# Kernel optimization log

Hardware: AMD Instinct MI355X
Metric: run time of the kernel (lower is better)

## Reference

```python
import jax, jax.numpy as jnp
import numpy as np

# model dims
B_, S_, D_ = 2, 2048, 1024
D_STATE, EXPAND, HEADDIM, CHUNK, NGROUPS = 128, 2, 64, 64, 1
D_INNER = EXPAND * D_
NHEADS = D_INNER // HEADDIM  # 32 ssd heads
D_PROJ = 2 * D_INNER + 2 * NGROUPS * D_STATE + NHEADS  # 4384
H_, KV_, HD_ = 16, 4, 64  # attention heads / kv heads / head dim
ROPE_DIMS = 16
MLP_DIM = int(3.0 * D_)


def _rmsnorm(x, w=None, eps=1e-5):
    y = x * jax.lax.rsqrt(jnp.mean(x * x, axis=-1, keepdims=True) + eps)
    return y * w if w is not None else y


def _layernorm(x, w, b, eps=1e-5):
    m = jnp.mean(x, axis=-1, keepdims=True)
    v = jnp.mean((x - m) ** 2, axis=-1, keepdims=True)
    return (x - m) * jax.lax.rsqrt(v + eps) * w + b


def _segsum(x):
    # (..., T) -> (..., T, T) lower-tri cumulative sums, -inf above diag
    T = x.shape[-1]
    i = jnp.arange(T)
    xx = jnp.where(i[:, None] > i[None, :], jnp.broadcast_to(x[..., None], x.shape + (T,)), 0.0)
    s = jnp.cumsum(xx, axis=-2)
    return jnp.where(i[:, None] >= i[None, :], s, -jnp.inf)


def _ssd_chunked(x, A, B, C, chunk):
    # x:(b,s,h,p) A:(b,s,h) B,C:(b,s,g,n)
    b, s, h, p = x.shape
    g, n = B.shape[2], B.shape[3]
    if g < h:
        B = jnp.repeat(B, h // g, axis=2)
        C = jnp.repeat(C, h // g, axis=2)
    c = s // chunk
    x = x.reshape(b, c, chunk, h, p)
    A = A.reshape(b, c, chunk, h).transpose(0, 3, 1, 2)  # b h c l
    B = B.reshape(b, c, chunk, h, n)
    C = C.reshape(b, c, chunk, h, n)
    L = jnp.exp(_segsum(A))
    Y_diag = jnp.einsum('bclhn,bcshn,bhcls,bcshp->bclhp', C, B, L, x)
    A_cum = jnp.cumsum(A, axis=-1)
    decay_states = jnp.exp(A_cum[..., -1:] - A_cum)
    states = jnp.einsum('bclhn,bhcl,bclhp->bchpn', B, decay_states, x)
    decay_chunk = jnp.exp(_segsum(jnp.pad(A_cum[..., -1], ((0, 0), (0, 0), (1, 0)))))
    new_states = jnp.einsum('bhzc,bchpn->bzhpn', decay_chunk[:, :, :c, 1:c + 1], states)
    Y_off = jnp.einsum('bclhn,bchpn,bhcl->bclhp', C, new_states, jnp.exp(A_cum))
    return (Y_diag + Y_off).reshape(b, s, h, p)


def _rope_cos_sin(s, rd, base=10000.0):
    inv = 1.0 / base ** (jnp.arange(0, rd, 2, dtype=jnp.float32) / rd)
    f = jnp.outer(jnp.arange(s, dtype=jnp.float32), inv)  # (s, rd/2)
    return jnp.cos(f)[None, :, None, :], jnp.sin(f)[None, :, None, :]


def _apply_rope(x, cos, sin, rd):
    xr, xp = x[..., :rd], x[..., rd:]
    half = rd // 2
    x1, x2 = xr[..., :half], xr[..., half:]
    xr = jnp.concatenate([x1 * cos + x2 * sin, -x1 * sin + x2 * cos], axis=-1)
    return jnp.concatenate([xr, xp], axis=-1)


def _mamba_block(x, mnorm_w, in_w, out_w, Dp, dt_b, A_log, Bn_w, Cn_w):
    b, s, _ = x.shape
    h = _rmsnorm(x, mnorm_w)
    zxbcdt = h @ in_w.T
    z, xs, Bc, Cc, dt = jnp.split(
        zxbcdt,
        [D_INNER, 2 * D_INNER, 2 * D_INNER + NGROUPS * D_STATE, 2 * D_INNER + 2 * NGROUPS * D_STATE],
        axis=-1)
    dt = jax.nn.softplus(dt + dt_b)  # (b,s,nheads)
    A = -jnp.exp(A_log)  # (nheads,)
    xs = xs.reshape(b, s, NHEADS, HEADDIM)
    Bc = _rmsnorm(Bc.reshape(b, s, NGROUPS, D_STATE), Bn_w)
    Cc = _rmsnorm(Cc.reshape(b, s, NGROUPS, D_STATE), Cn_w)
    y = _ssd_chunked(xs * dt[..., None], A[None, None, :] * dt, Bc, Cc, CHUNK)
    y = y + xs * Dp[None, None, :, None]
    y = y * jax.nn.silu(z).reshape(b, s, NHEADS, HEADDIM)
    return x + y.reshape(b, s, D_INNER) @ out_w.T


def _attn_block(x, ln1_w, ln1_b, cq_w, ck_w, cv_w, cproj_w, q_gain, ln2_w, ln2_b, fc_w, proj_w):
    b, s, d = x.shape
    h = _layernorm(x, ln1_w, ln1_b)
    q = (h @ cq_w.T).reshape(b, s, H_, HD_)
    k = (h @ ck_w.T).reshape(b, s, KV_, HD_)
    v = (h @ cv_w.T).reshape(b, s, KV_, HD_)
    eps = jnp.finfo(x.dtype).eps
    q = _rmsnorm(q, eps=eps)
    k = _rmsnorm(k, eps=eps)
    cos, sin = _rope_cos_sin(s, ROPE_DIMS)
    q = _apply_rope(q, cos, sin, ROPE_DIMS)
    k = _apply_rope(k, cos, sin, ROPE_DIMS)
    q = q * q_gain[None, None, :, None]
    rep = H_ // KV_
    k = jnp.repeat(k, rep, axis=2)
    v = jnp.repeat(v, rep, axis=2)
    scores = jnp.einsum('bqhd,bkhd->bhqk', q, k) / np.float32(np.sqrt(HD_))
    i = jnp.arange(s)
    scores = jnp.where(i[:, None] >= i[None, :], scores, -jnp.inf)
    w = jax.nn.softmax(scores, axis=-1)
    y = jnp.einsum('bhqk,bkhd->bqhd', w, v).reshape(b, s, d)
    x = x + y @ cproj_w.T
    h = _layernorm(x, ln2_w, ln2_b)
    return x + jax.nn.silu(h @ fc_w.T) @ proj_w.T


def setup_inputs() -> dict:
    key = jax.random.key(0)
    ks = jax.random.split(key, 16)
    rn = lambda k, shp, sc=0.02: (jax.random.normal(k, shp, dtype=jnp.float32) * sc)
    return {
        'x': jax.random.normal(ks[0], (B_, S_, D_), dtype=jnp.float32),
        'mnorm_w': jnp.ones((D_,), jnp.float32),
        'in_proj_w': rn(ks[1], (D_PROJ, D_)),
        'out_proj_w': rn(ks[2], (D_, D_INNER)),
        'D_param': jnp.ones((NHEADS,), jnp.float32),
        'dt_bias': rn(ks[3], (NHEADS,), 0.1),
        'A_log': jnp.log(0.5 + jax.random.uniform(ks[4], (NHEADS,), dtype=jnp.float32) * 0.5),
        'Bn_w': jnp.ones((D_STATE,), jnp.float32),
        'Cn_w': jnp.ones((D_STATE,), jnp.float32),
        'ln1_w': jnp.ones((D_,), jnp.float32),
        'ln1_b': jnp.zeros((D_,), jnp.float32),
        'cq_w': rn(ks[5], (D_, D_)),
        'ck_w': rn(ks[6], (KV_ * HD_, D_)),
        'cv_w': rn(ks[7], (KV_ * HD_, D_)),
        'cproj_w': rn(ks[8], (D_, D_)),
        'q_gain': jnp.full((H_,), 5.25, jnp.float32),
        'ln2_w': jnp.ones((D_,), jnp.float32),
        'ln2_b': jnp.zeros((D_,), jnp.float32),
        'fc_w': rn(ks[9], (MLP_DIM, D_)),
        'proj_w': rn(ks[10], (D_, MLP_DIM)),
    }


def reference(x, mnorm_w, in_proj_w, out_proj_w, D_param, dt_bias, A_log, Bn_w, Cn_w,
              ln1_w, ln1_b, cq_w, ck_w, cv_w, cproj_w, q_gain, ln2_w, ln2_b, fc_w, proj_w):
    x = _mamba_block(x, mnorm_w, in_proj_w, out_proj_w, D_param, dt_bias, A_log, Bn_w, Cn_w)
    x = _attn_block(x, ln1_w, ln1_b, cq_w, ck_w, cv_w, cproj_w, q_gain, ln2_w, ln2_b, fc_w, proj_w)
    return x
```

## Files before the change

### kernel.cpp

```cpp
#include <hip/hip_runtime.h>
#include <hip/hip_bf16.h>
#include <math.h>

#define B_    2
#define S_    2048
#define D_    1024
#define DI    2048
#define NH    32
#define HD    64
#define DS    128
#define CH    64
#define NC    32
#define DP    4384
#define HATT  16
#define KVH   4
#define RD    16
#define MLP   3072
#define ROWS  (B_*S_)
#define PSB   (ROWS*288)

typedef __bf16 bf16;
typedef __bf16 bf16x8 __attribute__((ext_vector_type(8)));
typedef __bf16 bf16x4 __attribute__((ext_vector_type(4)));
typedef float  f32x4  __attribute__((ext_vector_type(4)));

__device__ __forceinline__ void async_copy16(const void* g, void* l) {
  __builtin_amdgcn_global_load_lds(
      (const __attribute__((address_space(1))) unsigned int*)g,
      (__attribute__((address_space(3))) unsigned int*)l, 16, 0, 0);
}

__device__ __forceinline__ float waveReduceSum(float v) {
#pragma unroll
  for (int off = 32; off > 0; off >>= 1) v += __shfl_down(v, off, 64);
  return v;
}

template<int NW>
__device__ __forceinline__ float blockReduceSum(float v, float* sh) {
  v = waveReduceSum(v);
  int lane = threadIdx.x & 63, wid = threadIdx.x >> 6;
  if (lane == 0) sh[wid] = v;
  __syncthreads();
  float s = 0.f;
#pragma unroll
  for (int i = 0; i < NW; i++) s += sh[i];
  __syncthreads();
  return s;
}

struct CastSeg { const float* src; bf16* dst; int nval; int ntot; int blk0; };
struct CastArgs { CastSeg seg[8]; };

__global__ __launch_bounds__(256) void castw_all(CastArgs a) {
  int blk = blockIdx.x;
  int si = 0;
#pragma unroll
  for (int i = 1; i < 8; i++) if (blk >= a.seg[i].blk0) si = i;
  CastSeg s = a.seg[si];
  int i = ((blk - s.blk0) * 256 + threadIdx.x) * 4;
  if (i >= s.ntot) return;
  float4 v = {0.f, 0.f, 0.f, 0.f};
  if (i < s.nval) v = *(const float4*)(s.src + i);
  bf16x4 o;
  o[0] = (bf16)v.x; o[1] = (bf16)v.y; o[2] = (bf16)v.z; o[3] = (bf16)v.w;
  *(bf16x4*)(s.dst + i) = o;
}

__global__ __launch_bounds__(256) void rmsnorm_k(const float* __restrict__ x,
                                                 const float* __restrict__ w,
                                                 bf16* __restrict__ y, int n) {
  __shared__ float sh[4];
  size_t row = blockIdx.x;
  const float* xr = x + row * n;
  bf16* yr = y + row * n;
  float ss = 0.f;
  for (int i = threadIdx.x; i < n; i += 256) { float v = xr[i]; ss += v * v; }
  ss = blockReduceSum<4>(ss, sh);
  float inv = rsqrtf(ss / n + 1e-5f);
  for (int i = threadIdx.x; i < n; i += 256) yr[i] = (bf16)(xr[i] * inv * w[i]);
}

template<int ACT, typename OT>
__global__ __launch_bounds__(256) void gemm_mfma(const bf16* __restrict__ A,
                                                 const bf16* __restrict__ W,
                                                 const float* __restrict__ R,
                                                 OT* __restrict__ C,
                                                 int M, int N, int K) {
  __shared__ bf16 lds[3 * 8192];
  int tid = threadIdx.x, lane = tid & 63, wave = tid >> 6;
  int mt = M >> 7;
  int bid = blockIdx.x;
  int bm = (bid % mt) * 128, bn = (bid / mt) * 128;
  const bf16* gA0 = A + (size_t)(bm + wave * 32 + (lane >> 2)) * K + (lane & 3) * 8;
  const bf16* gA1 = gA0 + (size_t)16 * K;
  const bf16* gW0 = W + (size_t)(bn + wave * 32 + (lane >> 2)) * K + (lane & 3) * 8;
  const bf16* gW1 = gW0 + (size_t)16 * K;
  int sA = wave * 1024;
  int fr = lane & 15, fq = lane >> 4;
  int wm = wave >> 1, wn = wave & 1;
  int rdA = (wm * 64 + fr) * 32 + fq * 8;
  int rdW = (wn * 64 + fr) * 32 + fq * 8;
  f32x4 acc[4][4] = {};
  {
    bf16* bA = lds + sA;
    bf16* bW = lds + 4096 + sA;
    async_copy16(gA0, bA);  async_copy16(gA1, bA + 512);
    async_copy16(gW0, bW);  async_copy16(gW1, bW + 512);
  }
  int cur = 0, nxt = 1;
  int nsteps = K >> 5;
  for (int t = 0; t < nsteps; t++) {
    if (t + 1 < nsteps) {
      int off = (t + 1) * 32;
      bf16* bA = lds + nxt * 8192 + sA;
      bf16* bW = lds + nxt * 8192 + 4096 + sA;
      async_copy16(gA0 + off, bA);  async_copy16(gA1 + off, bA + 512);
      async_copy16(gW0 + off, bW);  async_copy16(gW1 + off, bW + 512);
      asm volatile("s_waitcnt vmcnt(4)" ::: "memory");
    } else {
      asm volatile("s_waitcnt vmcnt(0)" ::: "memory");
    }
    __builtin_amdgcn_sched_barrier(0);
    __builtin_amdgcn_s_barrier();
    __builtin_amdgcn_sched_barrier(0);
    const bf16* cA = lds + cur * 8192;
    const bf16* cW = cA + 4096;
    bf16x8 af[4], bfr[4];
#pragma unroll
    for (int mi = 0; mi < 4; mi++) af[mi] = *(const bf16x8*)(cA + rdA + mi * 512);
#pragma unroll
    for (int ni = 0; ni < 4; ni++) bfr[ni] = *(const bf16x8*)(cW + rdW + ni * 512);
    __builtin_amdgcn_s_setprio(1);
#pragma unroll
    for (int mi = 0; mi < 4; mi++)
#pragma unroll
      for (int ni = 0; ni < 4; ni++)
        acc[mi][ni] = __builtin_amdgcn_mfma_f32_16x16x32_bf16(af[mi], bfr[ni], acc[mi][ni], 0, 0, 0);
    __builtin_amdgcn_s_setprio(0);
    cur = nxt; nxt = nxt + 1; if (nxt == 3) nxt = 0;
  }
#pragma unroll
  for (int mi = 0; mi < 4; mi++) {
    int row = bm + wm * 64 + mi * 16 + fq * 4;
#pragma unroll
    for (int ni = 0; ni < 4; ni++) {
      int col = bn + wn * 64 + ni * 16 + fr;
      if (col < N) {
#pragma unroll
        for (int r = 0; r < 4; r++) {
          float v = acc[mi][ni][r];
          if (ACT == 1) v = v / (1.f + __expf(-v));
          if (R) v += R[(size_t)(row + r) * N + col];
          C[(size_t)(row + r) * N + col] = (OT)v;
        }
      }
    }
  }
}

__global__ __launch_bounds__(256) void gemm_sk(const bf16* __restrict__ A,
                                               const bf16* __restrict__ W,
                                               bf16* __restrict__ P,
                                               int M, int N, int K, int kchunk) {
  __shared__ bf16 lds[3 * 8192];
  int tid = threadIdx.x, lane = tid & 63, wave = tid >> 6;
  int mt = M >> 7;
  int bid = blockIdx.x;
  int bm = (bid % mt) * 128, bn = (bid / mt) * 128;
  int ks = blockIdx.z;
  int kbeg = ks * kchunk;
  const bf16* gA0 = A + (size_t)(bm + wave * 32 + (lane >> 2)) * K + kbeg + (lane & 3) * 8;
  const bf16* gA1 = gA0 + (size_t)16 * K;
  const bf16* gW0 = W + (size_t)(bn + wave * 32 + (lane >> 2)) * K + kbeg + (lane & 3) * 8;
  const bf16* gW1 = gW0 + (size_t)16 * K;
  int sA = wave * 1024;
  int fr = lane & 15, fq = lane >> 4;
  int wm = wave >> 1, wn = wave & 1;
  int rdA = (wm * 64 + fr) * 32 + fq * 8;
  int rdW = (wn * 64 + fr) * 32 + fq * 8;
  f32x4 acc[4][4] = {};
  {
    bf16* bA = lds + sA;
    bf16* bW = lds + 4096 + sA;
    async_copy16(gA0, bA);  async_copy16(gA1, bA + 512);
    async_copy16(gW0, bW);  async_copy16(gW1, bW + 512);
  }
  int cur = 0, nxt = 1;
  int nsteps = kchunk >> 5;
  for (int t = 0; t < nsteps; t++) {
    if (t + 1 < nsteps) {
      int off = (t + 1) * 32;
      bf16* bA = lds + nxt * 8192 + sA;
      bf16* bW = lds + nxt * 8192 + 4096 + sA;
      async_copy16(gA0 + off, bA);  async_copy16(gA1 + off, bA + 512);
      async_copy16(gW0 + off, bW);  async_copy16(gW1 + off, bW + 512);
      asm volatile("s_waitcnt vmcnt(4)" ::: "memory");
    } else {
      asm volatile("s_waitcnt vmcnt(0)" ::: "memory");
    }
    __builtin_amdgcn_sched_barrier(0);
    __builtin_amdgcn_s_barrier();
    __builtin_amdgcn_sched_barrier(0);
    const bf16* cA = lds + cur * 8192;
    const bf16* cW = cA + 4096;
    bf16x8 af[4], bfr[4];
#pragma unroll
    for (int mi = 0; mi < 4; mi++) af[mi] = *(const bf16x8*)(cA + rdA + mi * 512);
#pragma unroll
    for (int ni = 0; ni < 4; ni++) bfr[ni] = *(const bf16x8*)(cW + rdW + ni * 512);
    __builtin_amdgcn_s_setprio(1);
#pragma unroll
    for (int mi = 0; mi < 4; mi++)
#pragma unroll
      for (int ni = 0; ni < 4; ni++)
        acc[mi][ni] = __builtin_amdgcn_mfma_f32_16x16x32_bf16(af[mi], bfr[ni], acc[mi][ni], 0, 0, 0);
    __builtin_amdgcn_s_setprio(0);
    cur = nxt; nxt = nxt + 1; if (nxt == 3) nxt = 0;
  }
  bf16* Pp = P + (size_t)ks * M * N;
#pragma unroll
  for (int mi = 0; mi < 4; mi++) {
    int row = bm + wm * 64 + mi * 16 + fq * 4;
#pragma unroll
    for (int ni = 0; ni < 4; ni++) {
      int col = bn + wn * 64 + ni * 16 + fr;
#pragma unroll
      for (int r = 0; r < 4; r++)
        Pp[(size_t)(row + r) * N + col] = (bf16)acc[mi][ni][r];
    }
  }
}

__global__ __launch_bounds__(256) void reduce_ln2(const bf16* __restrict__ p0,
                                                  const bf16* __restrict__ p1,
                                                  const float* __restrict__ res,
                                                  const float* __restrict__ w,
                                                  const float* __restrict__ b,
                                                  float* __restrict__ xo,
                                                  bf16* __restrict__ ho) {
  __shared__ float sh[4];
  size_t o = (size_t)blockIdx.x * 1024;
  int i = threadIdx.x * 4;
  bf16x4 a = *(const bf16x4*)(p0 + o + i);
  bf16x4 c = *(const bf16x4*)(p1 + o + i);
  f32x4 rv = *(const f32x4*)(res + o + i);
  f32x4 v;
  float s = 0.f, s2 = 0.f;
#pragma unroll
  for (int j = 0; j < 4; j++) {
    v[j] = (float)a[j] + (float)c[j] + rv[j];
    s += v[j]; s2 += v[j] * v[j];
  }
  s  = blockReduceSum<4>(s,  sh);
  s2 = blockReduceSum<4>(s2, sh);
  float mean = s / 1024.f;
  float var  = s2 / 1024.f - mean * mean;
  float inv  = rsqrtf(var + 1e-5f);
  f32x4 wv = *(const f32x4*)(w + i);
  f32x4 bv = *(const f32x4*)(b + i);
  *(f32x4*)(xo + o + i) = v;
  bf16x4 hv;
#pragma unroll
  for (int j = 0; j < 4; j++) hv[j] = (bf16)((v[j] - mean) * inv * wv[j] + bv[j]);
  *(bf16x4*)(ho + o + i) = hv;
}

__global__ __launch_bounds__(256) void reduce_out3(const bf16* __restrict__ p0,
                                                   const bf16* __restrict__ p1,
                                                   const bf16* __restrict__ p2,
                                                   const float* __restrict__ res,
                                                   float* __restrict__ out) {
  int i = (blockIdx.x * 256 + threadIdx.x) * 4;
  bf16x4 a = *(const bf16x4*)(p0 + i);
  bf16x4 c = *(const bf16x4*)(p1 + i);
  bf16x4 d = *(const bf16x4*)(p2 + i);
  f32x4 v = *(const f32x4*)(res + i);
#pragma unroll
  for (int j = 0; j < 4; j++) v[j] += (float)a[j] + (float)c[j] + (float)d[j];
  *(f32x4*)(out + i) = v;
}

__global__ __launch_bounds__(256) void reduce_qkv(const bf16* __restrict__ P,
                                                  const float* __restrict__ q_gain,
                                                  bf16* __restrict__ q,
                                                  bf16* __restrict__ k,
                                                  bf16* __restrict__ v) {
  __shared__ float buf[1536];
  size_t row = blockIdx.x;
  size_t o = row * 1536;
  const bf16* p0 = P + o;
  const bf16* p1 = P + (size_t)ROWS * 1536 + o;
  int tid = threadIdx.x;
  for (int i = tid; i < 384; i += 256) {
    bf16x4 a = *(const bf16x4*)(p0 + i * 4);
    bf16x4 c = *(const bf16x4*)(p1 + i * 4);
    f32x4 vv;
#pragma unroll
    for (int j = 0; j < 4; j++) vv[j] = (float)a[j] + (float)c[j];
    *(f32x4*)(buf + i * 4) = vv;
  }
  __syncthreads();
  int lane = tid & 63, w = tid >> 6;
  int s = (int)(row & (S_ - 1));
  int ri = lane & 7;
  float rinv = __expf(-(float)ri * (0.125f * 9.210340371976184f));
  float ang = (float)s * rinv;
  float cs = cosf(ang), sn = sinf(ang);
#pragma unroll
  for (int j = 0; j < 6; j++) {
    int hh = w * 6 + j;
    float val = buf[hh * 64 + lane];
    if (hh < 20) {
      float ss = val * val;
#pragma unroll
      for (int off = 32; off > 0; off >>= 1) ss += __shfl_xor(ss, off, 64);
      val *= rsqrtf(ss / 64.f + 1.1920929e-7f);
      float other = __shfl_xor(val, 8, 64);
      float res = val;
      if (lane < RD) res = (lane < 8) ? (val * cs + other * sn) : (val * cs - other * sn);
      if (hh < 16) {
        res *= q_gain[hh];
        q[row * (HATT * HD) + hh * HD + lane] = (bf16)res;
      } else {
        k[row * (KVH * HD) + (hh - 16) * HD + lane] = (bf16)res;
      }
    } else {
      v[row * (KVH * HD) + (hh - 20) * HD + lane] = (bf16)val;
    }
  }
}

__global__ __launch_bounds__(512, 2) void gemm256_inproj(const bf16* __restrict__ A,
                                                         const bf16* __restrict__ W,
                                                         bf16* __restrict__ zt,
                                                         bf16* __restrict__ xt,
                                                         bf16* __restrict__ bcdtP) {
  __shared__ bf16 lds[3 * 16384];
  int tid = threadIdx.x;
  int lane = tid & 63, w = tid >> 6;
  int fr = lane & 15, fq = lane >> 4;
  int rdswz = (fq ^ (fr & 3)) * 8;
  int sswz = (lane & 3) ^ ((lane >> 2) & 3);
  int bid = blockIdx.x;
  if (bid < 256) {
    int sb = (bid & 7) * 32 + (bid >> 3);
    int bm = (sb & 15) * 256;
    int bn = (sb >> 4) * 256;
    int wm = w >> 2, wn = w & 3;
    int srow = w * 32 + (lane >> 2);
    const bf16* gA = A + (size_t)(bm + srow) * 1024 + sswz * 8;
    const bf16* gW = W + (size_t)(bn + srow) * 1024 + sswz * 8;
    int sbase = w * 1024;
    f32x4 acc[8][4] = {};
    {
      bf16* bA = lds + sbase;
      bf16* bB = lds + 8192 + sbase;
      async_copy16(gA, bA);
      async_copy16(gA + 16 * 1024, bA + 512);
      async_copy16(gW, bB);
      async_copy16(gW + 16 * 1024, bB + 512);
    }
    int cur = 0, nxt = 1;
    for (int t = 0; t < 32; t++) {
      if (t + 1 < 32) {
        const bf16* ga = gA + (t + 1) * 32;
        const bf16* gw = gW + (t + 1) * 32;
        bf16* bA = lds + nxt * 16384 + sbase;
        bf16* bB = lds + nxt * 16384 + 8192 + sbase;
        async_copy16(ga, bA);
        async_copy16(ga + 16 * 1024, bA + 512);
        async_copy16(gw, bB);
        async_copy16(gw + 16 * 1024, bB + 512);
        asm volatile("s_waitcnt vmcnt(4)" ::: "memory");
      } else {
        asm volatile("s_waitcnt vmcnt(0)" ::: "memory");
      }
      __builtin_amdgcn_sched_barrier(0);
      __builtin_amdgcn_s_barrier();
      __builtin_amdgcn_sched_barrier(0);
      const bf16* cA = lds + cur * 16384;
      const bf16* cB = cA + 8192;
      bf16x8 af[8], bfv[4];
#pragma unroll
      for (int mi = 0; mi < 8; mi++)
        af[mi] = *(const bf16x8*)(cA + (wm * 128 + mi * 16 + fr) * 32 + rdswz);
#pragma unroll
      for (int ni = 0; ni < 4; ni++)
        bfv[ni] = *(const bf16x8*)(cB + (wn * 64 + ni * 16 + fr) * 32 + rdswz);
      __builtin_amdgcn_s_setprio(1);
#pragma unroll
      for (int mi = 0; mi < 8; mi++)
#pragma unroll
        for (int ni = 0; ni < 4; ni++)
          acc[mi][ni] = __builtin_amdgcn_mfma_f32_16x16x32_bf16(af[mi], bfv[ni], acc[mi][ni], 0, 0, 0);
      __builtin_amdgcn_s_setprio(0);
      cur = nxt; nxt = nxt + 1; if (nxt == 3) nxt = 0;
    }
    bf16* base = (bn < 2048) ? zt : xt;
    int bq = bm >> 11, bmS = bm & 2047;
    bf16* Ts = lds;
#pragma unroll 1
    for (int g = 0; g < 4; g++) {
      __syncthreads();
      if (wn == g) {
#pragma unroll
        for (int mi = 0; mi < 8; mi++)
#pragma unroll
          for (int ni = 0; ni < 4; ni++) {
            bf16x4 o;
#pragma unroll
            for (int r = 0; r < 4; r++) o[r] = (bf16)acc[mi][ni][r];
            *(bf16x4*)(Ts + (ni * 16 + fr) * 264 + wm * 128 + mi * 16 + fq * 4) = o;
          }
      }
      __syncthreads();
      int hh = ((bn & 2047) + g * 64) >> 6;
      bf16* dst = base + ((size_t)(bq * NH + hh) * HD) * S_ + bmS;
#pragma unroll
      for (int i = 0; i < 4; i++) {
        int idx = tid + i * 512;
        int p = idx >> 5, sc = (idx & 31) * 8;
        *(bf16x8*)(dst + (size_t)p * S_ + sc) = *(const bf16x8*)(Ts + p * 264 + sc);
      }
    }
  } else {
    int lb = bid - 256;
    int ks = lb / 96;
    int pos = lb - ks * 96;
    int bm = (pos & 31) * 128;
    int bn = 4096 + (pos >> 5) * 128;
    int kbeg = ks * 512;
    int wm = w >> 1, wn = w & 1;
    int srow = w * 16 + (lane >> 2);
    const bf16* gA = A + (size_t)(bm + srow) * 1024 + kbeg + sswz * 8;
    const bf16* gW = W + (size_t)(bn + srow) * 1024 + kbeg + sswz * 8;
    int sbase = w * 512;
    f32x4 acc[2][4] = {};
    {
      async_copy16(gA, lds + sbase);
      async_copy16(gW, lds + 4096 + sbase);
    }
    int cur = 0, nxt = 1;
    for (int t = 0; t < 16; t++) {
      if (t + 1 < 16) {
        async_copy16(gA + (t + 1) * 32, lds + nxt * 8192 + sbase);
        async_copy16(gW + (t + 1) * 32, lds + nxt * 8192 + 4096 + sbase);
        asm volatile("s_waitcnt vmcnt(2)" ::: "memory");
      } else {
        asm volatile("s_waitcnt vmcnt(0)" ::: "memory");
      }
      __builtin_amdgcn_sched_barrier(0);
      __builtin_amdgcn_s_barrier();
      __builtin_amdgcn_sched_barrier(0);
      const bf16* cA = lds + cur * 8192;
      const bf16* cB = cA + 4096;
      bf16x8 af[2], bfv[4];
#pragma unroll
      for (int mi = 0; mi < 2; mi++)
        af[mi] = *(const bf16x8*)(cA + (wm * 32 + mi * 16 + fr) * 32 + rdswz);
#pragma unroll
      for (int ni = 0; ni < 4; ni++)
        bfv[ni] = *(const bf16x8*)(cB + (wn * 64 + ni * 16 + fr) * 32 + rdswz);
#pragma unroll
      for (int mi = 0; mi < 2; mi++)
#pragma unroll
        for (int ni = 0; ni < 4; ni++)
          acc[mi][ni] = __builtin_amdgcn_mfma_f32_16x16x32_bf16(af[mi], bfv[ni], acc[mi][ni], 0, 0, 0);
      cur = nxt; nxt = nxt + 1; if (nxt == 3) nxt = 0;
    }
    bf16* dst = bcdtP + (size_t)ks * PSB;
#pragma unroll
    for (int mi = 0; mi < 2; mi++) {
      int row = bm + wm * 32 + mi * 16 + fq * 4;
#pragma unroll
      for (int ni = 0; ni < 4; ni++) {
        int col = bn + wn * 64 + ni * 16 + fr;
        if (col < 4384) {
#pragma unroll
          for (int r = 0; r < 4; r++)
            dst[(size_t)(row + r) * 288 + (col - 4096)] = (bf16)acc[mi][ni][r];
        }
      }
    }
  }
}

__global__ __launch_bounds__(256) void t64(const bf16* __restrict__ in, bf16* __restrict__ out,
                                           int istr, size_t io, size_t oo, int n_nt) {
  __shared__ bf16 T[64 * 72];
  int bid = blockIdx.x;
  int st = bid & 31;
  int nt = (bid >> 5) % n_nt;
  int outer = bid / (32 * n_nt);
  const bf16* ip = in + outer * io + (size_t)st * 64 * istr + nt * 64;
  int tid = threadIdx.x;
#pragma unroll
  for (int i = 0; i < 2; i++) {
    int cid = tid + i * 256; int s = cid >> 3, pc = (cid & 7) * 8;
    *(bf16x8*)(T + s * 72 + pc) = *(const bf16x8*)(ip + (size_t)s * istr + pc);
  }
  __syncthreads();
  bf16* op = out + outer * oo + (size_t)nt * 64 * 2048 + st * 64;
#pragma unroll
  for (int i = 0; i < 2; i++) {
    int cid = tid + i * 256; int p = cid >> 3, sc = (cid & 7) * 8;
    bf16x8 o;
#pragma unroll
    for (int j = 0; j < 8; j++) o[j] = T[(sc + j) * 72 + p];
    *(bf16x8*)(op + (size_t)p * 2048 + sc) = o;
  }
}

__global__ __launch_bounds__(64) void ssd_prep(const bf16* __restrict__ bcdtP,
                                               const float* __restrict__ dt_bias,
                                               const float* __restrict__ A_log,
                                               float* __restrict__ dt_c,
                                               float* __restrict__ ddc,
                                               float* __restrict__ ac_c,
                                               float* __restrict__ T_out) {
  int bid = blockIdx.x;
  int c = bid % NC, hh = (bid / NC) % NH, b = bid / (NC * NH);
  int l = threadIdx.x;
  size_t row = (size_t)b * S_ + c * 64 + l;
  float raw = (float)bcdtP[row * 288 + 256 + hh]
            + (float)bcdtP[(size_t)PSB + row * 288 + 256 + hh] + dt_bias[hh];
  float dtv = (raw > 20.f) ? raw : log1pf(__expf(raw));
  float a = -__expf(A_log[hh]) * dtv;
  float ps = a;
#pragma unroll
  for (int off = 1; off < 64; off <<= 1) {
    float t = __shfl_up(ps, off, 64);
    if (l >= off) ps += t;
  }
  float a63 = __shfl(ps, 63, 64);
  size_t o = ((size_t)b * NH + hh) * S_ + c * 64 + l;
  dt_c[o] = dtv;
  ac_c[o] = ps;
  ddc[o] = __expf(a63 - ps) * dtv;
  if (l == 63) T_out[(b * NH + hh) * NC + c] = ps;
}

__global__ __launch_bounds__(128) void bc_norm(const bf16* __restrict__ bcdtP,
                                               const float* __restrict__ Bw,
                                               const float* __restrict__ Cw,
                                               bf16* __restrict__ Bn,
                                               bf16* __restrict__ Cn) {
  __shared__ float shb[2], shc[2];
  size_t row = blockIdx.x;
  int i = threadIdx.x;
  float bv = (float)bcdtP[row * 288 + i] + (float)bcdtP[(size_t)PSB + row * 288 + i];
  float cv = (float)bcdtP[row * 288 + 128 + i] + (float)bcdtP[(size_t)PSB + row * 288 + 128 + i];
  float sb = waveReduceSum(bv * bv);
  float sc = waveReduceSum(cv * cv);
  int lane = threadIdx.x & 63, wid = threadIdx.x >> 6;
  if (lane == 0) { shb[wid] = sb; shc[wid] = sc; }
  __syncthreads();
  float tb = shb[0] + shb[1];
  float tc = shc[0] + shc[1];
  Bn[row * DS + i] = (bf16)(bv * rsqrtf(tb / DS + 1e-5f) * Bw[i]);
  Cn[row * DS + i] = (bf16)(cv * rsqrtf(tc / DS + 1e-5f) * Cw[i]);
}

__global__ __launch_bounds__(256) void ssd_states(const bf16* __restrict__ Xt,
                                                  const bf16* __restrict__ Btr,
                                                  const float* __restrict__ ddc,
                                                  bf16* __restrict__ states) {
  __shared__ bf16 Xs[64 * 72];
  __shared__ bf16 Bs[128 * 72];
  int bid = blockIdx.x;
  int h = bid % NH;
  int c = (bid / NH) % NC;
  int b = bid / (NH * NC);
  int tid = threadIdx.x, lane = tid & 63, w = tid >> 6;
  int fr = lane & 15, fq = lane >> 4;
  const size_t xbase = (size_t)(b * NH + h) * HD * S_ + c * 64;
  const size_t dbase = (size_t)(b * NH + h) * S_ + c * 64;
#pragma unroll
  for (int i = 0; i < 2; i++) {
    int cid = tid + i * 256; int p = cid >> 3, sc = (cid & 7) * 8;
    bf16x8 xv = *(const bf16x8*)(Xt + xbase + (size_t)p * S_ + sc);
    f32x4 d0 = *(const f32x4*)(ddc + dbase + sc);
// ... 152 lines not shown
  for (int pt = 0; pt < 4; pt++)
#pragma unroll
    for (int ks = 0; ks < 4; ks++)
      acc[pt] = __builtin_amdgcn_mfma_f32_16x16x32_bf16(ca[ks],
                  *(const bf16x8*)(BNs + (pt * 16 + fr) * 136 + ks * 32 + fq * 8), acc[pt], 0, 0, 0);
  float dph = Dp[h];
#pragma unroll
  for (int pt = 0; pt < 4; pt++) {
    int p = pt * 16 + fr;
    size_t tb = (xbase + (size_t)p * S_) + w * 16 + fq * 4;
    bf16x4 xs4 = *(const bf16x4*)(Xt + tb);
    bf16x4 z4  = *(const bf16x4*)(Zt + tb);
#pragma unroll
    for (int r = 0; r < 4; r++) {
      int l = w * 16 + fq * 4 + r;
      float yv = acc[pt][r] + (float)xs4[r] * dph;
      float z = (float)z4[r];
      yv *= z / (1.f + __expf(-z));
      ybf[((row0 + l) * NH + h) * HD + p] = (bf16)yv;
    }
  }
}

#define KSTR 72
#define PSTR 72
__global__ __launch_bounds__(256) void attn_mfma(const bf16* __restrict__ q,
                                                 const bf16* __restrict__ k,
                                                 const bf16* __restrict__ vtr,
                                                 bf16* __restrict__ Po,
                                                 float* __restrict__ Ls) {
  __shared__ bf16 Ks[64 * KSTR];
  __shared__ bf16 Vs[64 * KSTR];
  __shared__ bf16 Pl[4][32 * PSTR];
  int c = 39 - blockIdx.x;
  int g = (c < 4) ? 0 : (c < 12) ? 1 : (c < 24) ? 2 : 3;
  int gbase = (g == 0) ? 0 : (g == 1) ? 4 : (g == 2) ? 12 : 24;
  int d = c - gbase;
  int qt = 4 * g + d / (g + 1);
  int sk = d % (g + 1);
  int h = blockIdx.y, b = blockIdx.z;
  int kvh = h >> 2;
  int tid = threadIdx.x, lane = tid & 63, w = tid >> 6;
  int fr = lane & 15, fq = lane >> 4;
  const float SC = 0.18033688011112042f;
  const float M2 = 62.0f;
  int kt0 = sk * 8;
  int ktend = min(kt0 + 8, 2 * qt + 2);
  int qbase = qt * 128 + w * 32;
  int qmaxw = qbase + 31;
  bf16x8 bq[2][2];
#pragma unroll
  for (int qc = 0; qc < 2; qc++)
#pragma unroll
    for (int ks = 0; ks < 2; ks++)
      bq[qc][ks] = *(const bf16x8*)(q + (size_t)(b * S_ + qbase + qc * 16 + fr) * (HATT * HD)
                                      + h * HD + ks * 32 + fq * 8);
  int sr = tid >> 3, sc8 = (tid & 7) * 8;
  const bf16* kg = k + ((size_t)(b * S_) + sr) * (KVH * HD) + kvh * HD + sc8;
  const bf16* vg = vtr + ((size_t)(b * KVH + kvh) * HD + sr) * S_ + sc8;
  bf16x8 krg0, krg1, vrg0, vrg1;
  {
    const bf16* kp = kg + (size_t)kt0 * 64 * (KVH * HD);
    const bf16* vp = vg + (size_t)kt0 * 64;
    krg0 = *(const bf16x8*)(kp);
    krg1 = *(const bf16x8*)(kp + (size_t)32 * (KVH * HD));
    vrg0 = *(const bf16x8*)(vp);
    vrg1 = *(const bf16x8*)(vp + (size_t)32 * S_);
  }
  float lsum[2] = {0.f, 0.f};
  f32x4 yacc[2][4] = {};
  bf16* Plw = Pl[w];
  for (int kt = kt0; kt < ktend; kt++) {
    __syncthreads();
    *(bf16x8*)(&Ks[sr * KSTR + sc8]) = krg0;
    *(bf16x8*)(&Ks[(sr + 32) * KSTR + sc8]) = krg1;
    *(bf16x8*)(&Vs[sr * KSTR + sc8]) = vrg0;
    *(bf16x8*)(&Vs[(sr + 32) * KSTR + sc8]) = vrg1;
    __syncthreads();
    if ((kt + 1) < ktend) {
      const bf16* kp = kg + (size_t)(kt + 1) * 64 * (KVH * HD);
      const bf16* vp = vg + (size_t)(kt + 1) * 64;
      krg0 = *(const bf16x8*)(kp);
      krg1 = *(const bf16x8*)(kp + (size_t)32 * (KVH * HD));
      vrg0 = *(const bf16x8*)(vp);
      vrg1 = *(const bf16x8*)(vp + (size_t)32 * S_);
    }
    if (kt * 64 <= qmaxw) {
      bool nomask = (kt * 64 + 63) <= qbase;
      if (nomask) {
#pragma unroll
        for (int mi = 0; mi < 4; mi++) {
          const bf16* krow = &Ks[(mi * 16 + fr) * KSTR];
          bf16x8 ak0 = *(const bf16x8*)(krow + fq * 8);
          bf16x8 ak1 = *(const bf16x8*)(krow + 32 + fq * 8);
#pragma unroll
          for (int qc = 0; qc < 2; qc++) {
            f32x4 s = {};
            s = __builtin_amdgcn_mfma_f32_16x16x32_bf16(ak0, bq[qc][0], s, 0, 0, 0);
            s = __builtin_amdgcn_mfma_f32_16x16x32_bf16(ak1, bq[qc][1], s, 0, 0, 0);
            bf16x4 pk;
#pragma unroll
            for (int r = 0; r < 4; r++) {
              float p = __builtin_amdgcn_exp2f(s[r] * SC - M2);
              lsum[qc] += p;
              pk[r] = (bf16)p;
            }
            *(bf16x4*)(Plw + (qc * 16 + fr) * PSTR + mi * 16 + fq * 4) = pk;
          }
        }
      } else {
#pragma unroll
        for (int mi = 0; mi < 4; mi++) {
          int s0 = kt * 64 + mi * 16;
          if (s0 > qmaxw) {
            bf16x4 zz = {};
#pragma unroll
            for (int qc = 0; qc < 2; qc++)
              *(bf16x4*)(Plw + (qc * 16 + fr) * PSTR + mi * 16 + fq * 4) = zz;
          } else {
            const bf16* krow = &Ks[(mi * 16 + fr) * KSTR];
            bf16x8 ak0 = *(const bf16x8*)(krow + fq * 8);
            bf16x8 ak1 = *(const bf16x8*)(krow + 32 + fq * 8);
#pragma unroll
            for (int qc = 0; qc < 2; qc++) {
              f32x4 s = {};
              s = __builtin_amdgcn_mfma_f32_16x16x32_bf16(ak0, bq[qc][0], s, 0, 0, 0);
              s = __builtin_amdgcn_mfma_f32_16x16x32_bf16(ak1, bq[qc][1], s, 0, 0, 0);
              int qq = qbase + qc * 16 + fr;
              bf16x4 pk;
#pragma unroll
              for (int r = 0; r < 4; r++) {
                int sp = s0 + fq * 4 + r;
                float p = (sp <= qq) ? __builtin_amdgcn_exp2f(s[r] * SC - M2) : 0.f;
                lsum[qc] += p;
                pk[r] = (bf16)p;
              }
              *(bf16x4*)(Plw + (qc * 16 + fr) * PSTR + mi * 16 + fq * 4) = pk;
            }
          }
        }
      }
#pragma unroll
      for (int ks2 = 0; ks2 < 2; ks2++) {
        bf16x8 bp[2];
#pragma unroll
        for (int qc = 0; qc < 2; qc++)
          bp[qc] = *(const bf16x8*)(Plw + (qc * 16 + fr) * PSTR + ks2 * 32 + fq * 8);
#pragma unroll
        for (int pi = 0; pi < 4; pi++) {
          bf16x8 av = *(const bf16x8*)(&Vs[(pi * 16 + fr) * KSTR + ks2 * 32 + fq * 8]);
#pragma unroll
          for (int qc = 0; qc < 2; qc++)
            yacc[qc][pi] = __builtin_amdgcn_mfma_f32_16x16x32_bf16(av, bp[qc], yacc[qc][pi], 0, 0, 0);
        }
      }
    }
  }
#pragma unroll
  for (int qc = 0; qc < 2; qc++) {
    lsum[qc] += __shfl_xor(lsum[qc], 16, 64);
    lsum[qc] += __shfl_xor(lsum[qc], 32, 64);
    int qrow = qt * 128 + w * 32 + qc * 16 + fr;
    if (fq == 0)
      Ls[((size_t)(b * 16 + h) * 2048 + qrow) * 4 + sk] = lsum[qc];
    bf16* pop = Po + ((((size_t)(b * 16 + h) * 16 + qt) * 4 + sk) * 128
                       + w * 32 + qc * 16 + fr) * 64 + fq * 4;
#pragma unroll
    for (int pi = 0; pi < 4; pi++) {
      bf16x4 o;
#pragma unroll
      for (int r = 0; r < 4; r++) o[r] = (bf16)yacc[qc][pi][r];
      *(bf16x4*)(pop + pi * 16) = o;
    }
  }
}

__global__ __launch_bounds__(256) void attn_red(const bf16* __restrict__ Po,
                                                const float* __restrict__ Ls,
                                                bf16* __restrict__ y2) {
  int row = blockIdx.x;
  int b = row >> 11;
  int qrow = row & 2047;
  int qt = qrow >> 7, r = qrow & 127;
  int nch = (qt >> 2) + 1;
  int t = threadIdx.x;
  int h = t >> 4, e4 = (t & 15) << 2;
  const float* lp = Ls + ((size_t)(b * 16 + h) * 2048 + qrow) * 4;
  float ls = 0.f;
  f32x4 acc = {};
  for (int sk = 0; sk < nch; sk++) {
    ls += lp[sk];
    const bf16* pp = Po + ((((size_t)(b * 16 + h) * 16 + qt) * 4 + sk) * 128 + r) * 64 + e4;
    bf16x4 v = *(const bf16x4*)(pp);
#pragma unroll
    for (int j = 0; j < 4; j++) acc[j] += (float)v[j];
  }
  float inv = 1.f / ls;
  bf16x4 o;
#pragma unroll
  for (int j = 0; j < 4; j++) o[j] = (bf16)(acc[j] * inv);
  *(bf16x4*)(y2 + (size_t)row * 1024 + h * 64 + e4) = o;
}

constexpr size_t OFF_WIN  = 0;
constexpr size_t OFF_WOUT = 9175040;
constexpr size_t OFF_WQKV = 13369344;
constexpr size_t OFF_WCP  = 16515072;
constexpr size_t OFF_WFC  = 18612224;
constexpr size_t OFF_WPR  = 24903680;
constexpr size_t OFF_HBF  = 31195136;
constexpr size_t OFF_BCDT = 39583744;
constexpr size_t OFF_XT   = 41943040;
constexpr size_t OFF_ZT   = 58720256;
constexpr size_t OFF_DTC  = 75497472;
constexpr size_t OFF_DDC  = 76546048;
constexpr size_t OFF_ACC  = 77594624;
constexpr size_t OFF_T    = 78643200;
constexpr size_t OFF_BN   = 78651392;
constexpr size_t OFF_CN   = 79699968;
constexpr size_t OFF_BTR  = 80748544;
constexpr size_t OFF_ST   = 81797120;
constexpr size_t OFF_YBF  = 148905984;
constexpr size_t OFF_X1   = 165683200;
constexpr size_t OFF_P    = OFF_ST;
constexpr size_t OFF_PO   = OFF_ST;
constexpr size_t OFF_LS   = OFF_BCDT;
constexpr size_t OFF_QB   = OFF_XT;
constexpr size_t OFF_KB   = OFF_XT + 8388608;
constexpr size_t OFF_VB   = OFF_XT + 10485760;
constexpr size_t OFF_VTR  = OFF_XT + 12582912;
constexpr size_t OFF_Y2   = OFF_ZT;
constexpr size_t OFF_X2   = 50331648;
constexpr size_t OFF_MLP  = 132128768;

extern "C" void kernel_launch(void* const* d_in, const int* in_sizes, int n_in,
                              void* d_out, int out_size, void* d_ws, size_t ws_size,
                              hipStream_t stream) {
  (void)in_sizes; (void)n_in; (void)out_size; (void)ws_size;
  const float* x        = (const float*)d_in[0];
  const float* mnorm_w  = (const float*)d_in[1];
  const float* in_w     = (const float*)d_in[2];
  const float* out_w    = (const float*)d_in[3];
  const float* Dp       = (const float*)d_in[4];
  const float* dt_bias  = (const float*)d_in[5];
  const float* A_log    = (const float*)d_in[6];
  const float* Bn_w     = (const float*)d_in[7];
  const float* Cn_w     = (const float*)d_in[8];
  const float* ln1_w    = (const float*)d_in[9];
  const float* ln1_b    = (const float*)d_in[10];
  const float* cq_w     = (const float*)d_in[11];
  const float* ck_w     = (const float*)d_in[12];
  const float* cv_w     = (const float*)d_in[13];
  const float* cproj_w  = (const float*)d_in[14];
  const float* q_gain   = (const float*)d_in[15];
  const float* ln2_w    = (const float*)d_in[16];
  const float* ln2_b    = (const float*)d_in[17];
  const float* fc_w     = (const float*)d_in[18];
  const float* proj_w   = (const float*)d_in[19];
  float* out = (float*)d_out;
  char* W8 = (char*)d_ws;

  bf16* w_in   = (bf16*)(W8 + OFF_WIN);
  bf16* w_out  = (bf16*)(W8 + OFF_WOUT);
  bf16* w_qkv  = (bf16*)(W8 + OFF_WQKV);
  bf16* w_cp   = (bf16*)(W8 + OFF_WCP);
  bf16* w_fc   = (bf16*)(W8 + OFF_WFC);
  bf16* w_pr   = (bf16*)(W8 + OFF_WPR);
  bf16* h_bf   = (bf16*)(W8 + OFF_HBF);
  bf16* bcdtP  = (bf16*)(W8 + OFF_ST);
  bf16* Xt     = (bf16*)(W8 + OFF_XT);
  bf16* Zt     = (bf16*)(W8 + OFF_ZT);
  float* dt_c  = (float*)(W8 + OFF_DTC);
  float* ddc   = (float*)(W8 + OFF_DDC);
  float* ac_c  = (float*)(W8 + OFF_ACC);
  float* Tb    = (float*)(W8 + OFF_T);
  bf16* Bn     = (bf16*)(W8 + OFF_BN);
  bf16* Cn     = (bf16*)(W8 + OFF_CN);
  bf16* Btr    = (bf16*)(W8 + OFF_BTR);
  bf16* st     = (bf16*)(W8 + OFF_ST);
  bf16* ybf    = (bf16*)(W8 + OFF_YBF);
  float* x1    = (float*)(W8 + OFF_X1);
  bf16* Pbuf   = (bf16*)(W8 + OFF_P);
  bf16* Po     = (bf16*)(W8 + OFF_PO);
  float* Ls    = (float*)(W8 + OFF_LS);
  bf16* qbf    = (bf16*)(W8 + OFF_QB);
  bf16* kbf    = (bf16*)(W8 + OFF_KB);
  bf16* vbf    = (bf16*)(W8 + OFF_VB);
  bf16* vtr    = (bf16*)(W8 + OFF_VTR);
  bf16* y2     = (bf16*)(W8 + OFF_Y2);
  float* x2    = (float*)(W8 + OFF_X2);
  bf16* mlp    = (bf16*)(W8 + OFF_MLP);

  CastArgs ca;
  ca.seg[0] = { in_w,    w_in,            4489216, 4587520, 0     };
  ca.seg[1] = { out_w,   w_out,           2097152, 2097152, 4480  };
  ca.seg[2] = { cq_w,    w_qkv,           1048576, 1048576, 6528  };
  ca.seg[3] = { ck_w,    w_qkv + 1048576,  262144,  262144, 7552  };
  ca.seg[4] = { cv_w,    w_qkv + 1310720,  262144,  262144, 7808  };
  ca.seg[5] = { cproj_w, w_cp,            1048576, 1048576, 8064  };
  ca.seg[6] = { fc_w,    w_fc,            3145728, 3145728, 9088  };
  ca.seg[7] = { proj_w,  w_pr,            3145728, 3145728, 12160 };
  castw_all<<<15232, 256, 0, stream>>>(ca);

  const size_t PS  = (size_t)ROWS * 1024;

  rmsnorm_k<<<ROWS, 256, 0, stream>>>(x, mnorm_w, h_bf, D_);
  gemm256_inproj<<<448, 512, 0, stream>>>(h_bf, w_in, Zt, Xt, bcdtP);
  ssd_prep<<<B_ * NH * NC, 64, 0, stream>>>(bcdtP, dt_bias, A_log, dt_c, ddc, ac_c, Tb);
  bc_norm<<<ROWS, 128, 0, stream>>>(bcdtP, Bn_w, Cn_w, Bn, Cn);
  t64<<<2 * 2 * 32, 256, 0, stream>>>(Bn, Btr, 128, (size_t)2048 * 128, (size_t)128 * 2048, 2);
  ssd_states<<<B_ * NC * NH, 256, 0, stream>>>(Xt, Btr, ddc, st);
  ssd_scan<<<B_ * NH * 8, 256, 0, stream>>>(st, Tb);
  ssd_out<<<B_ * NC * NH, 256, 0, stream>>>(Cn, Bn, Xt, Zt, dt_c, ac_c, st, Dp, ybf);
  gemm_sk<<<dim3(32 * 8, 1, 2), 256, 0, stream>>>(ybf, w_out, Pbuf, ROWS, D_, DI, 1024);
  reduce_ln2<<<ROWS, 256, 0, stream>>>(Pbuf, Pbuf + PS, x, ln1_w, ln1_b, x1, h_bf);

  gemm_sk<<<dim3(32 * 12, 1, 2), 256, 0, stream>>>(h_bf, w_qkv, Pbuf, ROWS, 1536, D_, 512);
  reduce_qkv<<<ROWS, 256, 0, stream>>>(Pbuf, q_gain, qbf, kbf, vbf);
  t64<<<2 * 4 * 32, 256, 0, stream>>>(vbf, vtr, 256, (size_t)2048 * 256, (size_t)256 * 2048, 4);
  attn_mfma<<<dim3(40, HATT, B_), 256, 0, stream>>>(qbf, kbf, vtr, Po, Ls);
  attn_red<<<ROWS, 256, 0, stream>>>(Po, Ls, y2);
  gemm_sk<<<dim3(32 * 8, 1, 2), 256, 0, stream>>>(y2, w_cp, Pbuf, ROWS, D_, D_, 512);
  reduce_ln2<<<ROWS, 256, 0, stream>>>(Pbuf, Pbuf + PS, x1, ln2_w, ln2_b, x2, h_bf);

  gemm_mfma<1, bf16><<<32 * 24, 256, 0, stream>>>(h_bf, w_fc, nullptr, mlp, ROWS, MLP, D_);
  gemm_sk<<<dim3(32 * 8, 1, 3), 256, 0, stream>>>(mlp, w_pr, Pbuf, ROWS, D_, MLP, 1024);
  reduce_out3<<<ROWS, 256, 0, stream>>>(Pbuf, Pbuf + PS, Pbuf + 2 * PS, x2, out);
}
```

Before: 496.0 us.

## Replace 128x128 GEMMs with unified 256x256 split-K MFMA kernel with swizzled LDS

Replaces the separate 128x128-tile gemm_mfma and gemm_sk kernels with a single 256x256-tile, 512-thread gemm256 kernel. The new kernel uses an XOR-swizzled LDS layout and remaps block IDs across the 8 XCDs. Split-K factors change: the out-proj, c_proj and MLP down-proj GEMMs now use 4 partials, and the MLP up-proj has SiLU fused and no split-K. The reductions are updated to sum 4 partials. The larger tiles aim for more operand reuse per load and fewer launches per wave. The cost is 96KB of LDS per block, which limits occupancy, and a larger partial buffer that must be allocated with enough room.

```diff
diff --git a/kernel.cpp b/kernel.cpp
--- a/kernel.cpp
+++ b/kernel.cpp
@@ -81,120 +81,52 @@
   for (int i = threadIdx.x; i < n; i += 256) yr[i] = (bf16)(xr[i] * inv * w[i]);
 }
 
-template<int ACT, typename OT>
-__global__ __launch_bounds__(256) void gemm_mfma(const bf16* __restrict__ A,
-                                                 const bf16* __restrict__ W,
-                                                 const float* __restrict__ R,
-                                                 OT* __restrict__ C,
-                                                 int M, int N, int K) {
-  __shared__ bf16 lds[3 * 8192];
-  int tid = threadIdx.x, lane = tid & 63, wave = tid >> 6;
-  int mt = M >> 7;
+template<int ACT>
+__global__ __launch_bounds__(512, 2) void gemm256(const bf16* __restrict__ A,
+                                                  const bf16* __restrict__ W,
+                                                  bf16* __restrict__ P,
+                                                  int N, int K, int kchunk, int nwg) {
+  __shared__ bf16 lds[3 * 16384];
+  int tid = threadIdx.x;
+  int lane = tid & 63, w = tid >> 6;
+  int fr = lane & 15, fq = lane >> 4;
+  int rdswz = (fq ^ (fr & 3)) * 8;
+  int sswz = (lane & 3) ^ ((lane >> 2) & 3);
   int bid = blockIdx.x;
-  int bm = (bid % mt) * 128, bn = (bid / mt) * 128;
-  const bf16* gA0 = A + (size_t)(bm + wave * 32 + (lane >> 2)) * K + (lane & 3) * 8;
-  const bf16* gA1 = gA0 + (size_t)16 * K;
-  const bf16* gW0 = W + (size_t)(bn + wave * 32 + (lane >> 2)) * K + (lane & 3) * 8;
-  const bf16* gW1 = gW0 + (size_t)16 * K;
-  int sA = wave * 1024;
-  int fr = lane & 15, fq = lane >> 4;
-  int wm = wave >> 1, wn = wave & 1;
-  int rdA = (wm * 64 + fr) * 32 + fq * 8;
-  int rdW = (wn * 64 + fr) * 32 + fq * 8;
-  f32x4 acc[4][4] = {};
+  int cpx = nwg >> 3;
+  bid = (bid & 7) * cpx + (bid >> 3);
+  int bm = (bid & 15) * 256;
+  int rest = bid >> 4;
+  int nt = N >> 8;
+  int bn = (rest % nt) * 256;
+  int ks = rest / nt;
+  int kbeg = ks * kchunk;
+  int wm = w >> 2, wn = w & 3;
+  int srow = w * 32 + (lane >> 2);
+  const bf16* gA = A + (size_t)(bm + srow) * K + kbeg + sswz * 8;
+  const bf16* gW = W + (size_t)(bn + srow) * K + kbeg + sswz * 8;
+  int sbase = w * 1024;
+  f32x4 acc[8][4] = {};
   {
-    bf16* bA = lds + sA;
-    bf16* bW = lds + 4096 + sA;
-    async_copy16(gA0, bA);  async_copy16(gA1, bA + 512);
-    async_copy16(gW0, bW);  async_copy16(gW1, bW + 512);
-  }
-  int cur = 0, nxt = 1;
-  int nsteps = K >> 5;
-  for (int t = 0; t < nsteps; t++) {
-    if (t + 1 < nsteps) {
-      int off = (t + 1) * 32;
-      bf16* bA = lds + nxt * 8192 + sA;
-      bf16* bW = lds + nxt * 8192 + 4096 + sA;
-      async_copy16(gA0 + off, bA);  async_copy16(gA1 + off, bA + 512);
-      async_copy16(gW0 + off, bW);  async_copy16(gW1 + off, bW + 512);
-      asm volatile("s_waitcnt vmcnt(4)" ::: "memory");
-    } else {
-      asm volatile("s_waitcnt vmcnt(0)" ::: "memory");
-    }
-    __builtin_amdgcn_sched_barrier(0);
-    __builtin_amdgcn_s_barrier();
-    __builtin_amdgcn_sched_barrier(0);
-    const bf16* cA = lds + cur * 8192;
-    const bf16* cW = cA + 4096;
-    bf16x8 af[4], bfr[4];
-#pragma unroll
-    for (int mi = 0; mi < 4; mi++) af[mi] = *(const bf16x8*)(cA + rdA + mi * 512);
-#pragma unroll
-    for (int ni = 0; ni < 4; ni++) bfr[ni] = *(const bf16x8*)(cW + rdW + ni * 512);
-    __builtin_amdgcn_s_setprio(1);
-#pragma unroll
-    for (int mi = 0; mi < 4; mi++)
-#pragma unroll
-      for (int ni = 0; ni < 4; ni++)
-        acc[mi][ni] = __builtin_amdgcn_mfma_f32_16x16x32_bf16(af[mi], bfr[ni], acc[mi][ni], 0, 0, 0);
-    __builtin_amdgcn_s_setprio(0);
-    cur = nxt; nxt = nxt + 1; if (nxt == 3) nxt = 0;
-  }
-#pragma unroll
-  for (int mi = 0; mi < 4; mi++) {
-    int row = bm + wm * 64 + mi * 16 + fq * 4;
-#pragma unroll
-    for (int ni = 0; ni < 4; ni++) {
-      int col = bn + wn * 64 + ni * 16 + fr;
-      if (col < N) {
-#pragma unroll
-        for (int r = 0; r < 4; r++) {
-          float v = acc[mi][ni][r];
-          if (ACT == 1) v = v / (1.f + __expf(-v));
-          if (R) v += R[(size_t)(row + r) * N + col];
-          C[(size_t)(row + r) * N + col] = (OT)v;
-        }
-      }
-    }
-  }
-}
-
-__global__ __launch_bounds__(256) void gemm_sk(const bf16* __restrict__ A,
-                                               const bf16* __restrict__ W,
-                                               bf16* __restrict__ P,
-                                               int M, int N, int K, int kchunk) {
-  __shared__ bf16 lds[3 * 8192];
-  int tid = threadIdx.x, lane = tid & 63, wave = tid >> 6;
-  int mt = M >> 7;
-  int bid = blockIdx.x;
-  int bm = (bid % mt) * 128, bn = (bid / mt) * 128;
-  int ks = blockIdx.z;
-  int kbeg = ks * kchunk;
-  const bf16* gA0 = A + (size_t)(bm + wave * 32 + (lane >> 2)) * K + kbeg + (lane & 3) * 8;
-  const bf16* gA1 = gA0 + (size_t)16 * K;
-  const bf16* gW0 = W + (size_t)(bn + wave * 32 + (lane >> 2)) * K + kbeg + (lane & 3) * 8;
-  const bf16* gW1 = gW0 + (size_t)16 * K;
-  int sA = wave * 1024;
-  int fr = lane & 15, fq = lane >> 4;
-  int wm = wave >> 1, wn = wave & 1;
-  int rdA = (wm * 64 + fr) * 32 + fq * 8;
-  int rdW = (wn * 64 + fr) * 32 + fq * 8;
-  f32x4 acc[4][4] = {};
-  {
-    bf16* bA = lds + sA;
-    bf16* bW = lds + 4096 + sA;
-    async_copy16(gA0, bA);  async_copy16(gA1, bA + 512);
-    async_copy16(gW0, bW);  async_copy16(gW1, bW + 512);
+    bf16* bA = lds + sbase;
+    bf16* bB = lds + 8192 + sbase;
+    async_copy16(gA, bA);
+    async_copy16(gA + (size_t)16 * K, bA + 512);
+    async_copy16(gW, bB);
+    async_copy16(gW + (size_t)16 * K, bB + 512);
   }
   int cur = 0, nxt = 1;
   int nsteps = kchunk >> 5;
   for (int t = 0; t < nsteps; t++) {
     if (t + 1 < nsteps) {
-      int off = (t + 1) * 32;
-      bf16* bA = lds + nxt * 8192 + sA;
-      bf16* bW = lds + nxt * 8192 + 4096 + sA;
-      async_copy16(gA0 + off, bA);  async_copy16(gA1 + off, bA + 512);
-      async_copy16(gW0 + off, bW);  async_copy16(gW1 + off, bW + 512);
+      const bf16* ga = gA + (t + 1) * 32;
+      const bf16* gw = gW + (t + 1) * 32;
+      bf16* bA = lds + nxt * 16384 + sbase;
+      bf16* bB = lds + nxt * 16384 + 8192 + sbase;
+      async_copy16(ga, bA);
+      async_copy16(ga + (size_t)16 * K, bA + 512);
+      async_copy16(gw, bB);
+      async_copy16(gw + (size_t)16 * K, bB + 512);
       asm volatile("s_waitcnt vmcnt(4)" ::: "memory");
     } else {
       asm volatile("s_waitcnt vmcnt(0)" ::: "memory");
@@ -202,56 +134,61 @@
     __builtin_amdgcn_sched_barrier(0);
     __builtin_amdgcn_s_barrier();
     __builtin_amdgcn_sched_barrier(0);
-    const bf16* cA = lds + cur * 8192;
-    const bf16* cW = cA + 4096;
-    bf16x8 af[4], bfr[4];
-#pragma unroll
-    for (int mi = 0; mi < 4; mi++) af[mi] = *(const bf16x8*)(cA + rdA + mi * 512);
-#pragma unroll
-    for (int ni = 0; ni < 4; ni++) bfr[ni] = *(const bf16x8*)(cW + rdW + ni * 512);
+    const bf16* cA = lds + cur * 16384;
+    const bf16* cB = cA + 8192;
+    bf16x8 af[8], bfv[4];
+#pragma unroll
+    for (int mi = 0; mi < 8; mi++)
+      af[mi] = *(const bf16x8*)(cA + (wm * 128 + mi * 16 + fr) * 32 + rdswz);
+#pragma unroll
+    for (int ni = 0; ni < 4; ni++)
+      bfv[ni] = *(const bf16x8*)(cB + (wn * 64 + ni * 16 + fr) * 32 + rdswz);
     __builtin_amdgcn_s_setprio(1);
 #pragma unroll
-    for (int mi = 0; mi < 4; mi++)
+    for (int mi = 0; mi < 8; mi++)
 #pragma unroll
       for (int ni = 0; ni < 4; ni++)
-        acc[mi][ni] = __builtin_amdgcn_mfma_f32_16x16x32_bf16(af[mi], bfr[ni], acc[mi][ni], 0, 0, 0);
+        acc[mi][ni] = __builtin_amdgcn_mfma_f32_16x16x32_bf16(af[mi], bfv[ni], acc[mi][ni], 0, 0, 0);
     __builtin_amdgcn_s_setprio(0);
     cur = nxt; nxt = nxt + 1; if (nxt == 3) nxt = 0;
   }
-  bf16* Pp = P + (size_t)ks * M * N;
-#pragma unroll
-  for (int mi = 0; mi < 4; mi++) {
-    int row = bm + wm * 64 + mi * 16 + fq * 4;
+  bf16* Pp = P + (size_t)ks * ROWS * N;
+#pragma unroll
+  for (int mi = 0; mi < 8; mi++) {
+    int row = bm + wm * 128 + mi * 16 + fq * 4;
 #pragma unroll
     for (int ni = 0; ni < 4; ni++) {
       int col = bn + wn * 64 + ni * 16 + fr;
 #pragma unroll
-      for (int r = 0; r < 4; r++)
-        Pp[(size_t)(row + r) * N + col] = (bf16)acc[mi][ni][r];
-    }
-  }
-}
-
-__global__ __launch_bounds__(256) void reduce_ln2(const bf16* __restrict__ p0,
-                                                  const bf16* __restrict__ p1,
+      for (int r = 0; r < 4; r++) {
+        float v = acc[mi][ni][r];
+        if (ACT == 1) v = v / (1.f + __expf(-v));
+        Pp[(size_t)(row + r) * N + col] = (bf16)v;
+      }
+    }
+  }
+}
+
+__global__ __launch_bounds__(256) void reduce_ln4(const bf16* __restrict__ P,
                                                   const float* __restrict__ res,
                                                   const float* __restrict__ w,
                                                   const float* __restrict__ b,
                                                   float* __restrict__ xo,
                                                   bf16* __restrict__ ho) {
   __shared__ float sh[4];
+  const size_t PS4 = (size_t)ROWS * 1024;
   size_t o = (size_t)blockIdx.x * 1024;
   int i = threadIdx.x * 4;
-  bf16x4 a = *(const bf16x4*)(p0 + o + i);
-  bf16x4 c = *(const bf16x4*)(p1 + o + i);
-  f32x4 rv = *(const f32x4*)(res + o + i);
-  f32x4 v;
+  f32x4 v = *(const f32x4*)(res + o + i);
+#pragma unroll
+  for (int p = 0; p < 4; p++) {
+    bf16x4 a = *(const bf16x4*)(P + p * PS4 + o + i);
+#pragma unroll
+    for (int j = 0; j < 4; j++) v[j] += (float)a[j];
+  }
   float s = 0.f, s2 = 0.f;
 #pragma unroll
-  for (int j = 0; j < 4; j++) {
-    v[j] = (float)a[j] + (float)c[j] + rv[j];
-    s += v[j]; s2 += v[j] * v[j];
-  }
+  for (int j = 0; j < 4; j++) { s += v[j]; s2 += v[j] * v[j]; }
   s  = blockReduceSum<4>(s,  sh);
   s2 = blockReduceSum<4>(s2, sh);
   float mean = s / 1024.f;
@@ -266,18 +203,18 @@
   *(bf16x4*)(ho + o + i) = hv;
 }
 
-__global__ __launch_bounds__(256) void reduce_out3(const bf16* __restrict__ p0,
-                                                   const bf16* __restrict__ p1,
-                                                   const bf16* __restrict__ p2,
+__global__ __launch_bounds__(256) void reduce_out4(const bf16* __restrict__ P,
                                                    const float* __restrict__ res,
                                                    float* __restrict__ out) {
-  int i = (blockIdx.x * 256 + threadIdx.x) * 4;
-  bf16x4 a = *(const bf16x4*)(p0 + i);
-  bf16x4 c = *(const bf16x4*)(p1 + i);
-  bf16x4 d = *(const bf16x4*)(p2 + i);
+  const size_t PS4 = (size_t)ROWS * 1024;
+  size_t i = ((size_t)blockIdx.x * 256 + threadIdx.x) * 4;
   f32x4 v = *(const f32x4*)(res + i);
 #pragma unroll
-  for (int j = 0; j < 4; j++) v[j] += (float)a[j] + (float)c[j] + (float)d[j];
+  for (int p = 0; p < 4; p++) {
+    bf16x4 a = *(const bf16x4*)(P + p * PS4 + i);
+#pragma unroll
+    for (int j = 0; j < 4; j++) v[j] += (float)a[j];
+  }
   *(f32x4*)(out + i) = v;
 }
 
@@ -1036,8 +973,6 @@
   ca.seg[7] = { proj_w,  w_pr,            3145728, 3145728, 12160 };
   castw_all<<<15232, 256, 0, stream>>>(ca);
 
-  const size_t PS  = (size_t)ROWS * 1024;
-
   rmsnorm_k<<<ROWS, 256, 0, stream>>>(x, mnorm_w, h_bf, D_);
   gemm256_inproj<<<448, 512, 0, stream>>>(h_bf, w_in, Zt, Xt, bcdtP);
   ssd_prep<<<B_ * NH * NC, 64, 0, stream>>>(bcdtP, dt_bias, A_log, dt_c, ddc, ac_c, Tb);
@@ -1046,18 +981,18 @@
   ssd_states<<<B_ * NC * NH, 256, 0, stream>>>(Xt, Btr, ddc, st);
   ssd_scan<<<B_ * NH * 8, 256, 0, stream>>>(st, Tb);
   ssd_out<<<B_ * NC * NH, 256, 0, stream>>>(Cn, Bn, Xt, Zt, dt_c, ac_c, st, Dp, ybf);
-  gemm_sk<<<dim3(32 * 8, 1, 2), 256, 0, stream>>>(ybf, w_out, Pbuf, ROWS, D_, DI, 1024);
-  reduce_ln2<<<ROWS, 256, 0, stream>>>(Pbuf, Pbuf + PS, x, ln1_w, ln1_b, x1, h_bf);
-
-  gemm_sk<<<dim3(32 * 12, 1, 2), 256, 0, stream>>>(h_bf, w_qkv, Pbuf, ROWS, 1536, D_, 512);
+  gemm256<0><<<256, 512, 0, stream>>>(ybf, w_out, Pbuf, 1024, 2048, 512, 256);
+  reduce_ln4<<<ROWS, 256, 0, stream>>>(Pbuf, x, ln1_w, ln1_b, x1, h_bf);
+
+  gemm256<0><<<192, 512, 0, stream>>>(h_bf, w_qkv, Pbuf, 1536, 1024, 512, 192);
   reduce_qkv<<<ROWS, 256, 0, stream>>>(Pbuf, q_gain, qbf, kbf, vbf);
   t64<<<2 * 4 * 32, 256, 0, stream>>>(vbf, vtr, 256, (size_t)2048 * 256, (size_t)256 * 2048, 4);
   attn_mfma<<<dim3(40, HATT, B_), 256, 0, stream>>>(qbf, kbf, vtr, Po, Ls);
   attn_red<<<ROWS, 256, 0, stream>>>(Po, Ls, y2);
-  gemm_sk<<<dim3(32 * 8, 1, 2), 256, 0, stream>>>(y2, w_cp, Pbuf, ROWS, D_, D_, 512);
-  reduce_ln2<<<ROWS, 256, 0, stream>>>(Pbuf, Pbuf + PS, x1, ln2_w, ln2_b, x2, h_bf);
-
-  gemm_mfma<1, bf16><<<32 * 24, 256, 0, stream>>>(h_bf, w_fc, nullptr, mlp, ROWS, MLP, D_);
-  gemm_sk<<<dim3(32 * 8, 1, 3), 256, 0, stream>>>(mlp, w_pr, Pbuf, ROWS, D_, MLP, 1024);
-  reduce_out3<<<ROWS, 256, 0, stream>>>(Pbuf, Pbuf + PS, Pbuf + 2 * PS, x2, out);
-}
+  gemm256<0><<<256, 512, 0, stream>>>(y2, w_cp, Pbuf, 1024, 1024, 256, 256);
+  reduce_ln4<<<ROWS, 256, 0, stream>>>(Pbuf, x1, ln2_w, ln2_b, x2, h_bf);
+
+  gemm256<1><<<192, 512, 0, stream>>>(h_bf, w_fc, mlp, 3072, 1024, 1024, 192);
+  gemm256<0><<<256, 512, 0, stream>>>(mlp, w_pr, Pbuf, 1024, 3072, 768, 256);
+  reduce_out4<<<ROWS * 4 / 4, 256, 0, stream>>>(Pbuf, x2, out);
+}
```

After: 489.1 us. No clear change (-1.4%).
